# Performance work log

Hardware: AMD Instinct MI355X
Metric: run time of the kernel (lower is better)

Reference implementation:

```python
import jax, jax.numpy as jnp
import numpy as np

TOP_K = 2


def setup_inputs() -> dict:
    key = jax.random.key(0)
    ks = jax.random.split(key, 6)
    B, T, H, E, F = 2, 2048, 1024, 8, 4096
    s1 = 1.0 / np.sqrt(H)
    s2 = 1.0 / np.sqrt(F)
    return {
        "hidden_states": jax.random.normal(ks[0], (B, T, H), dtype=jnp.float32),
        "router_w": jax.random.normal(ks[1], (E, H), dtype=jnp.float32) * s1,
        "w1": jax.random.normal(ks[2], (E, H, F), dtype=jnp.float32) * s1,
        "b1": jnp.zeros((E, F), dtype=jnp.float32),
        "w2": jax.random.normal(ks[3], (E, F, H), dtype=jnp.float32) * s2,
        "b2": jnp.zeros((E, H), dtype=jnp.float32),
    }


def reference(hidden_states, router_w, w1, b1, w2, b2):
    # hidden_states: [B,T,H]; router_w: [E,H]; w1: [E,H,F]; w2: [E,F,H]
    E = router_w.shape[0]
    K = TOP_K
    dt = hidden_states.dtype

    # Router
    router_logits = jnp.einsum("bth,eh->bte", hidden_states, router_w)  # [B,T,E]
    topk_values, topk_indices = jax.lax.top_k(router_logits, K)         # [B,T,K]
    topk_weights = jax.nn.softmax(topk_values.astype(jnp.float32), axis=-1).astype(dt)

    # Dense all-expert MLP (module computes every expert on every token)
    h_mid = jax.nn.gelu(
        jnp.einsum("bth,ehf->btef", hidden_states, w1) + b1, approximate=False
    )  # [B,T,E,F]
    expert_outputs = jnp.einsum("btef,efh->bteh", h_mid, w2) + b2  # [B,T,E,H]

    # Gather top-K expert outputs and combine
    topk_out = jnp.take_along_axis(expert_outputs, topk_indices[..., None], axis=2)  # [B,T,K,H]
    mixed_output = jnp.sum(topk_out * topk_weights[..., None], axis=2)  # [B,T,H]

    # Load-balancing aux loss
    router_probs = jax.nn.softmax(router_logits.astype(jnp.float32), axis=-1)
    P = router_probs.mean(axis=(0, 1))                       # [E]
    hard = jax.nn.one_hot(topk_indices, E, dtype=jnp.float32)  # [B,T,K,E]
    f = hard.mean(axis=(0, 1, 2))                            # [E]
    aux_loss = jnp.float32(E) * jnp.sum(f * P)

    # concept_mat is None in a fresh module -> statement loss is exactly 0
    statement_loss = jnp.float32(0.0)
    return mixed_output, aux_loss, statement_loss
```

## Files before the change

kernel.cpp:

```cpp
#include <hip/hip_runtime.h>


typedef unsigned short ushort_t;
typedef __attribute__((ext_vector_type(4))) unsigned int u32x4;
typedef __attribute__((ext_vector_type(4))) unsigned short u16x4;
typedef __attribute__((ext_vector_type(4))) float f32x4;
typedef __attribute__((ext_vector_type(8))) __bf16 bf16x8;

#define NTOK 4096
#define HD   1024
#define FD   4096
#define NE   8
#define NKTOT 8192

__device__ __forceinline__ ushort_t f2bf(float f) {
  unsigned u = __builtin_bit_cast(unsigned, f);
  u += 0x7fffu + ((u >> 16) & 1u);
  return (ushort_t)(u >> 16);
}
__device__ __forceinline__ float bf2f(ushort_t u) {
  unsigned v = ((unsigned)u) << 16;
  return __builtin_bit_cast(float, v);
}
__device__ __forceinline__ bf16x8 frag_ld(const void* p) {
  u32x4 v = *reinterpret_cast<const u32x4*>(p);
  return __builtin_bit_cast(bf16x8, v);
}

#define GLOAD16(g, l) __builtin_amdgcn_global_load_lds(                         \
    (const __attribute__((address_space(1))) unsigned int*)(g),                 \
    (__attribute__((address_space(3))) unsigned int*)(l), 16, 0, 0)

#define WAITVM0() asm volatile("s_waitcnt vmcnt(0)" ::: "memory")
#define BARRIER() do { asm volatile("s_waitcnt lgkmcnt(0)" ::: "memory");       \
                       __builtin_amdgcn_s_barrier(); } while (0)

__global__ void init_k(int* counts) {
  if (threadIdx.x < NE) counts[threadIdx.x] = 0;
}

__global__ void tconv_k(const float* __restrict__ src, ushort_t* __restrict__ dst,
                        int R, int C) {
  __shared__ float tile[64][65];
  const size_t zb = (size_t)blockIdx.z * R * C;
  const int r0 = blockIdx.y * 64, c0 = blockIdx.x * 64;
  const int tid = threadIdx.x;
  const int rl = tid >> 4, c4 = (tid & 15) * 4;
#pragma unroll
  for (int i = 0; i < 4; ++i) {
    const int r = rl + i * 16;
    const f32x4 v = *reinterpret_cast<const f32x4*>(src + zb + (size_t)(r0 + r) * C + c0 + c4);
    tile[r][c4 + 0] = v.x; tile[r][c4 + 1] = v.y;
    tile[r][c4 + 2] = v.z; tile[r][c4 + 3] = v.w;
  }
  __syncthreads();
  const int rr0 = (tid & 15) * 4, ccl = tid >> 4;
#pragma unroll
  for (int i = 0; i < 4; ++i) {
    const int cc = ccl + i * 16;
    u16x4 o;
    o.x = f2bf(tile[rr0 + 0][cc]); o.y = f2bf(tile[rr0 + 1][cc]);
    o.z = f2bf(tile[rr0 + 2][cc]); o.w = f2bf(tile[rr0 + 3][cc]);
    *reinterpret_cast<u16x4*>(dst + zb + (size_t)(c0 + cc) * R + r0 + rr0) = o;
  }
}

__global__ void router_k(const float* __restrict__ x, const float* __restrict__ rw,
                         ushort_t* __restrict__ Xbf,
                         float* __restrict__ tokP, int* __restrict__ counts,
                         int* __restrict__ tk_e, int* __restrict__ tk_s,
                         float* __restrict__ tk_w) {
  const int w = threadIdx.x >> 6, l = threadIdx.x & 63;
  const int t = blockIdx.x * 4 + w;
  const float* xr = x + (size_t)t * HD;
  ushort_t* xo = Xbf + (size_t)t * HD;
  float acc[NE];
#pragma unroll
  for (int e = 0; e < NE; ++e) acc[e] = 0.f;
  for (int it = 0; it < HD / 64; ++it) {
    const int h = l + it * 64;
    const float xv = xr[h];
    xo[h] = f2bf(xv);
#pragma unroll
    for (int e = 0; e < NE; ++e) acc[e] = fmaf(xv, rw[e * HD + h], acc[e]);
  }
#pragma unroll
  for (int e = 0; e < NE; ++e) {
#pragma unroll
    for (int s = 32; s > 0; s >>= 1) acc[e] += __shfl_xor(acc[e], s, 64);
  }
  float m = acc[0];
#pragma unroll
  for (int e = 1; e < NE; ++e) m = fmaxf(m, acc[e]);
  float ssum = 0.f;
  float p[NE];
#pragma unroll
  for (int e = 0; e < NE; ++e) { p[e] = expf(acc[e] - m); ssum += p[e]; }
  const float inv = 1.f / ssum;
  if (l < NE) tokP[(size_t)t * NE + l] = p[l] * inv;

  if (l == 0) {
    int i0 = 0; float v0 = acc[0];
#pragma unroll
    for (int e = 1; e < NE; ++e) if (acc[e] > v0) { v0 = acc[e]; i0 = e; }
    int i1 = -1; float v1 = -3.4e38f;
#pragma unroll
    for (int e = 0; e < NE; ++e) if (e != i0 && acc[e] > v1) { v1 = acc[e]; i1 = e; }
    const float w0 = 1.f / (1.f + expf(v1 - v0));
    const int s0 = atomicAdd(&counts[i0], 1);
    const int s1 = atomicAdd(&counts[i1], 1);
    tk_e[2 * t] = i0;     tk_s[2 * t] = s0;     tk_w[2 * t] = w0;
    tk_e[2 * t + 1] = i1; tk_s[2 * t + 1] = s1; tk_w[2 * t + 1] = 1.f - w0;
  }
}

__global__ void finalize_k(const float* __restrict__ tokP, const int* __restrict__ counts,
                           int* __restrict__ offsets, float* __restrict__ out_tail) {
  __shared__ float red[16][8];
  const int tid = threadIdx.x;
  f32x4 a0 = {0.f, 0.f, 0.f, 0.f}, a1 = {0.f, 0.f, 0.f, 0.f};
#pragma unroll
  for (int k = 0; k < 4; ++k) {
    const float* p = tokP + ((size_t)tid * 4 + k) * 8;
    a0 += *reinterpret_cast<const f32x4*>(p);
    a1 += *reinterpret_cast<const f32x4*>(p + 4);
  }
#pragma unroll
  for (int s = 1; s < 64; s <<= 1) {
#pragma unroll
    for (int c = 0; c < 4; ++c) {
      a0[c] += __shfl_xor(a0[c], s, 64);
      a1[c] += __shfl_xor(a1[c], s, 64);
    }
  }
  if ((tid & 63) == 0) {
    const int wv = tid >> 6;
#pragma unroll
    for (int c = 0; c < 4; ++c) { red[wv][c] = a0[c]; red[wv][4 + c] = a1[c]; }
  }
  __syncthreads();
  if (tid == 0) {
    float P[8];
    for (int c = 0; c < 8; ++c) {
      float s = 0.f;
      for (int q = 0; q < 16; ++q) s += red[q][c];
      P[c] = s * (1.f / NTOK);
    }
    int off = 0; float aux = 0.f;
    for (int q = 0; q < NE; ++q) { offsets[q] = off; off += counts[q]; }
    for (int q = 0; q < NE; ++q) aux += ((float)counts[q] / (float)NKTOT) * P[q];
    out_tail[0] = (float)NE * aux;
    out_tail[1] = 0.f;
  }
}

__global__ void build_slots_k(const int* __restrict__ tk_e, const int* __restrict__ tk_s,
                              const int* __restrict__ offsets, int* __restrict__ slot_token) {
  const int i = blockIdx.x * 256 + threadIdx.x;
  const int e = tk_e[i];
  slot_token[offsets[e] + tk_s[i]] = i >> 1;
}

template <bool IS_G1>
__global__ __launch_bounds__(256, 4) void moe_gemm(
    const ushort_t* __restrict__ A, const ushort_t* __restrict__ BT,
    const float* __restrict__ bias,
    const int* __restrict__ counts, const int* __restrict__ offsets,
    const int* __restrict__ slot_token,
    ushort_t* __restrict__ midout, ushort_t* __restrict__ ybuf) {
  constexpr int KDF = IS_G1 ? HD : FD;
  constexpr int ND  = IS_G1 ? FD : HD;
  constexpr int NSTEP = IS_G1 ? 16 : 32;
  const int id = blockIdx.x;
  const int e = id & 7;
  const int q = id >> 3;
  const int ty = q % 10;
  const int r = q / 10;
  const int np = IS_G1 ? r : (r >> 1);
  const int ks = IS_G1 ? 0 : (r & 1);
  const int n0 = np * 128;
  const int KB = ks * 2048;
  const int cnt = counts[e];
  if (ty * 128 >= cnt) return;
  const int off = offsets[e];
  const int pos0 = off + ty * 128;
  const int rr = cnt - ty * 128;
  const int rows_rem = rr < 128 ? rr : 128;

  __shared__ __align__(16) ushort_t lds[16384];

  const int tid = threadIdx.x;
  const int w = tid >> 6, l = tid & 63;
  const int wr = w >> 1, wc = w & 1;

  const int sw = (((l & 7) ^ ((l >> 3) & 7)) << 4);
  const char* aptr[4];
  const char* bptr[4];
#pragma unroll
  for (int c = 0; c < 4; ++c) {
    const int row = c * 32 + w * 8 + (l >> 3);
    int pos = pos0 + row; if (pos > NKTOT - 1) pos = NKTOT - 1;
    const size_t ar = IS_G1 ? (size_t)slot_token[pos] : (size_t)pos;
    aptr[c] = (const char*)A + (ar * KDF + KB) * 2 + sw;
    const int rb = n0 + row;
    bptr[c] = (const char*)BT + (((size_t)e * ND + rb) * KDF + KB) * 2 + sw;
  }

  f32x4 acc[4][4] = {};

  for (int t = 0; t < NSTEP; ++t) {
#pragma unroll
    for (int c = 0; c < 4; ++c)
      GLOAD16(aptr[c] + t * 128, &lds[(c * 32 + w * 8) * 64]);
#pragma unroll
    for (int c = 0; c < 4; ++c)
      GLOAD16(bptr[c] + t * 128, &lds[8192 + (c * 32 + w * 8) * 64]);
    WAITVM0();
    BARRIER();
    {
      const int arow = wr * 64 + (l & 15);
      const int brow = wc * 64 + (l & 15);
      const int key = l & 7;
#pragma unroll
      for (int kk = 0; kk < 2; ++kk) {
        const int kc = kk * 4 + (l >> 4);
        bf16x8 afr[4];
#pragma unroll
        for (int mm = 0; mm < 4; ++mm)
          afr[mm] = frag_ld(&lds[(arow + mm * 16) * 64 + ((kc ^ key) << 3)]);
        __builtin_amdgcn_s_setprio(1);
#pragma unroll
        for (int nn = 0; nn < 4; ++nn) {
          const bf16x8 bfr =
              frag_ld(&lds[8192 + (brow + nn * 16) * 64 + ((kc ^ key) << 3)]);
#pragma unroll
          for (int mm = 0; mm < 4; ++mm)
            acc[mm][nn] = __builtin_amdgcn_mfma_f32_16x16x32_bf16(
                afr[mm], bfr, acc[mm][nn], 0, 0, 0);
        }
        __builtin_amdgcn_s_setprio(0);
      }
    }
    BARRIER();
  }

  {
    const int lr4 = (l >> 4) * 4, lc = l & 15;
#pragma unroll
    for (int nn = 0; nn < 4; ++nn) {
      const int col = wc * 64 + nn * 16 + lc;
      const float bv = IS_G1 ? bias[(size_t)e * FD + n0 + col] : 0.f;
#pragma unroll
      for (int mm = 0; mm < 4; ++mm) {
        const int rb = wr * 64 + mm * 16 + lr4;
#pragma unroll
        for (int j = 0; j < 4; ++j) {
          float v = acc[mm][nn][j] + bv;
          if (IS_G1) v = 0.5f * v * (1.0f + erff(v * 0.70710678118654752f));
          lds[(rb + j) * 128 + col] = f2bf(v);
        }
      }
    }
    BARRIER();
#pragma unroll
    for (int p = 0; p < 8; ++p) {
      const int idx = p * 2048 + tid * 8;
      const int row = idx >> 7;
      const int col = idx & 127;
      if (row < rows_rem) {
        const u32x4 v = *reinterpret_cast<const u32x4*>(&lds[idx]);
        if (IS_G1)
          *reinterpret_cast<u32x4*>(&midout[(size_t)(pos0 + row) * FD + n0 + col]) = v;
        else
          *reinterpret_cast<u32x4*>(
              &ybuf[((size_t)ks * NKTOT + pos0 + row) * HD + n0 + col]) = v;
      }
    }
  }
}

__global__ void combine_k(const ushort_t* __restrict__ ybuf, const int* __restrict__ tk_e,
                          const int* __restrict__ tk_s, const float* __restrict__ tk_w,
                          const int* __restrict__ offsets, const float* __restrict__ b2,
                          float* __restrict__ out) {
  const int t = blockIdx.x;
  const int e0 = tk_e[2 * t], e1 = tk_e[2 * t + 1];
  const size_t p0 = (size_t)offsets[e0] + tk_s[2 * t];
  const size_t p1 = (size_t)offsets[e1] + tk_s[2 * t + 1];
  const float w0 = tk_w[2 * t], w1v = tk_w[2 * t + 1];
  const int h = threadIdx.x * 4;
  f32x4 s0 = *reinterpret_cast<const f32x4*>(b2 + (size_t)e0 * HD + h);
  f32x4 s1 = *reinterpret_cast<const f32x4*>(b2 + (size_t)e1 * HD + h);
#pragma unroll
  for (int ks = 0; ks < 2; ++ks) {
    const u16x4 a = *reinterpret_cast<const u16x4*>(
        &ybuf[((size_t)ks * NKTOT + p0) * HD + h]);
    const u16x4 b = *reinterpret_cast<const u16x4*>(
        &ybuf[((size_t)ks * NKTOT + p1) * HD + h]);
    s0.x += bf2f(a.x); s0.y += bf2f(a.y); s0.z += bf2f(a.z); s0.w += bf2f(a.w);
    s1.x += bf2f(b.x); s1.y += bf2f(b.y); s1.z += bf2f(b.z); s1.w += bf2f(b.w);
  }
  f32x4 o = s0 * w0 + s1 * w1v;
  *reinterpret_cast<f32x4*>(out + (size_t)t * HD + h) = o;
}

extern "C" void kernel_launch(void* const* d_in, const int* in_sizes, int n_in,
                              void* d_out, int out_size, void* d_ws, size_t ws_size,
                              hipStream_t stream) {
  const float* x  = (const float*)d_in[0];
  const float* rw = (const float*)d_in[1];
  const float* w1 = (const float*)d_in[2];
  const float* b1 = (const float*)d_in[3];
  const float* w2 = (const float*)d_in[4];
  const float* b2 = (const float*)d_in[5];
  float* out = (float*)d_out;

  char* ws = (char*)d_ws;
  ushort_t* Xbf  = (ushort_t*)(ws + 0);
  ushort_t* W1T  = (ushort_t*)(ws + 8388608);
  ushort_t* W2T  = (ushort_t*)(ws + 75497472);
  ushort_t* midb = (ushort_t*)(ws + 142606336);
  ushort_t* ybuf = (ushort_t*)(ws + 8388608);
  char* sm = ws + 209715200;
  int*   counts  = (int*)(sm);
  int*   offsets = (int*)(sm + 64);
  float* tokP    = (float*)(sm + 128);
  int*   tk_e    = (int*)(sm + 128 + 131072);
  int*   tk_s    = (int*)(sm + 128 + 131072 + 32768);
  float* tk_w    = (float*)(sm + 128 + 131072 + 65536);
  int*   slot_token = (int*)(sm + 128 + 131072 + 98304);

  init_k<<<1, 64, 0, stream>>>(counts);
  tconv_k<<<dim3(64, 16, 8), 256, 0, stream>>>(w1, W1T, HD, FD);
  tconv_k<<<dim3(16, 64, 8), 256, 0, stream>>>(w2, W2T, FD, HD);
  router_k<<<1024, 256, 0, stream>>>(x, rw, Xbf, tokP, counts, tk_e, tk_s, tk_w);
  finalize_k<<<1, 1024, 0, stream>>>(tokP, counts, offsets, out + (size_t)NTOK * HD);
  build_slots_k<<<32, 256, 0, stream>>>(tk_e, tk_s, offsets, slot_token);
  moe_gemm<true><<<2560, 256, 0, stream>>>(
      Xbf, W1T, b1, counts, offsets, slot_token, midb, (ushort_t*)nullptr);
  moe_gemm<false><<<1280, 256, 0, stream>>>(
      midb, W2T, b2, counts, offsets, slot_token, (ushort_t*)nullptr, ybuf);
  combine_k<<<4096, 256, 0, stream>>>(ybuf, tk_e, tk_s, tk_w, offsets, b2, out);
}
```

Before: 414.5 us.

## Double-buffer LDS tiles with half-depth K steps in MoE GEMM

Splits the 32 KB LDS tile into two 16 KB buffers with a K-step of 32 instead of 64. The next tile's global-to-LDS loads are issued before computing on the current one, so memory latency overlaps with MFMA work and one barrier per step is dropped. The LDS layout changes from a swizzled row-major form to a k-chunk-major form in which each lane loads one row. Launch bounds are raised to 5 blocks per CU. The trade-offs are twice as many loop iterations, possible LDS bank conflicts from the new unswizzled layout, and register pressure from the higher occupancy target.

```diff
diff --git a/kernel.cpp b/kernel.cpp
--- a/kernel.cpp
+++ b/kernel.cpp
@@ -162,7 +162,7 @@
 }
 
 template <bool IS_G1>
-__global__ __launch_bounds__(256, 4) void moe_gemm(
+__global__ __launch_bounds__(256, 5) void moe_gemm(
     const ushort_t* __restrict__ A, const ushort_t* __restrict__ BT,
     const float* __restrict__ bias,
     const int* __restrict__ counts, const int* __restrict__ offsets,
@@ -170,7 +170,7 @@
     ushort_t* __restrict__ midout, ushort_t* __restrict__ ybuf) {
   constexpr int KDF = IS_G1 ? HD : FD;
   constexpr int ND  = IS_G1 ? FD : HD;
-  constexpr int NSTEP = IS_G1 ? 16 : 32;
+  constexpr int NSTEP = IS_G1 ? 32 : 64;
   const int id = blockIdx.x;
   const int e = id & 7;
   const int q = id >> 3;
@@ -193,54 +193,56 @@
   const int w = tid >> 6, l = tid & 63;
   const int wr = w >> 1, wc = w & 1;
 
-  const int sw = (((l & 7) ^ ((l >> 3) & 7)) << 4);
-  const char* aptr[4];
-  const char* bptr[4];
-#pragma unroll
-  for (int c = 0; c < 4; ++c) {
-    const int row = c * 32 + w * 8 + (l >> 3);
-    int pos = pos0 + row; if (pos > NKTOT - 1) pos = NKTOT - 1;
-    const size_t ar = IS_G1 ? (size_t)slot_token[pos] : (size_t)pos;
-    aptr[c] = (const char*)A + (ar * KDF + KB) * 2 + sw;
-    const int rb = n0 + row;
-    bptr[c] = (const char*)BT + (((size_t)e * ND + rb) * KDF + KB) * 2 + sw;
-  }
+  const int rhalf = w & 1;
+  const int kc0 = (w >> 1) * 2;
+  const int srow = rhalf * 64 + l;
+  int pos = pos0 + srow; if (pos > NKTOT - 1) pos = NKTOT - 1;
+  const size_t arG = IS_G1 ? (size_t)slot_token[pos] : (size_t)pos;
+  const char* ap = (const char*)A + (arG * KDF + KB) * 2 + kc0 * 16;
+  const char* bp = (const char*)BT + (((size_t)e * ND + n0 + srow) * KDF + KB) * 2 + kc0 * 16;
+  ushort_t* dA0 = &lds[kc0 * 1024 + rhalf * 512];
+  ushort_t* dB0 = &lds[8192 + kc0 * 1024 + rhalf * 512];
 
   f32x4 acc[4][4] = {};
 
+  auto stage = [&](int t, int buf) {
+    const int tb = t * 64;
+    GLOAD16(ap + tb,      dA0 + buf * 4096);
+    GLOAD16(ap + tb + 16, dA0 + buf * 4096 + 1024);
+    GLOAD16(bp + tb,      dB0 + buf * 4096);
+    GLOAD16(bp + tb + 16, dB0 + buf * 4096 + 1024);
+  };
+  auto compute = [&](int buf) {
+    const ushort_t* Ab = &lds[buf * 4096];
+    const ushort_t* Bb = &lds[8192 + buf * 4096];
+    const int kc = l >> 4;
+    const int arow = wr * 64 + (l & 15);
+    const int brow = wc * 64 + (l & 15);
+    bf16x8 afr[4];
+#pragma unroll
+    for (int mm = 0; mm < 4; ++mm)
+      afr[mm] = frag_ld(&Ab[kc * 1024 + (arow + mm * 16) * 8]);
+    __builtin_amdgcn_s_setprio(1);
+#pragma unroll
+    for (int nn = 0; nn < 4; ++nn) {
+      const bf16x8 bfr = frag_ld(&Bb[kc * 1024 + (brow + nn * 16) * 8]);
+#pragma unroll
+      for (int mm = 0; mm < 4; ++mm)
+        acc[mm][nn] = __builtin_amdgcn_mfma_f32_16x16x32_bf16(
+            afr[mm], bfr, acc[mm][nn], 0, 0, 0);
+    }
+    __builtin_amdgcn_s_setprio(0);
+  };
+
+  stage(0, 0);
+  WAITVM0();
+  BARRIER();
+
   for (int t = 0; t < NSTEP; ++t) {
-#pragma unroll
-    for (int c = 0; c < 4; ++c)
-      GLOAD16(aptr[c] + t * 128, &lds[(c * 32 + w * 8) * 64]);
-#pragma unroll
-    for (int c = 0; c < 4; ++c)
-      GLOAD16(bptr[c] + t * 128, &lds[8192 + (c * 32 + w * 8) * 64]);
+    if (t + 1 < NSTEP) stage(t + 1, (t + 1) & 1);
+    __builtin_amdgcn_sched_barrier(0);
+    compute(t & 1);
     WAITVM0();
-    BARRIER();
-    {
-      const int arow = wr * 64 + (l & 15);
-      const int brow = wc * 64 + (l & 15);
-      const int key = l & 7;
-#pragma unroll
-      for (int kk = 0; kk < 2; ++kk) {
-        const int kc = kk * 4 + (l >> 4);
-        bf16x8 afr[4];
-#pragma unroll
-        for (int mm = 0; mm < 4; ++mm)
-          afr[mm] = frag_ld(&lds[(arow + mm * 16) * 64 + ((kc ^ key) << 3)]);
-        __builtin_amdgcn_s_setprio(1);
-#pragma unroll
-        for (int nn = 0; nn < 4; ++nn) {
-          const bf16x8 bfr =
-              frag_ld(&lds[8192 + (brow + nn * 16) * 64 + ((kc ^ key) << 3)]);
-#pragma unroll
-          for (int mm = 0; mm < 4; ++mm)
-            acc[mm][nn] = __builtin_amdgcn_mfma_f32_16x16x32_bf16(
-                afr[mm], bfr, acc[mm][nn], 0, 0, 0);
-        }
-        __builtin_amdgcn_s_setprio(0);
-      }
-    }
     BARRIER();
   }
 
```

After: 575.3 us. +38.8%, slower.
